# Performance work log

Hardware: AMD Instinct MI355X
Metric: run time of the kernel (lower is better)

## Reference

```python
import jax, jax.numpy as jnp
import numpy as np

EPS = 1e-6  # mmdet bbox_overlaps eps


def _nearest_bev(boxes7):
    # boxes7: [N, 7] = (x, y, z, dx, dy, dz, yaw). LiDARInstance3DBoxes.nearest_bev:
    # limit yaw to [-pi/2, pi/2) via limit_period(yaw, 0.5, pi); if |yaw| > pi/4 swap dx/dy,
    # then return axis-aligned (x1, y1, x2, y2).
    x, y = boxes7[:, 0], boxes7[:, 1]
    dx, dy = boxes7[:, 3], boxes7[:, 4]
    yaw = boxes7[:, 6]
    pi = jnp.float32(np.pi)
    normed = jnp.abs(yaw - jnp.floor(yaw / pi + 0.5) * pi)
    swap = normed > pi / 4
    w = jnp.where(swap, dy, dx)
    h = jnp.where(swap, dx, dy)
    return jnp.stack([x - w / 2, y - h / 2, x + w / 2, y + h / 2], axis=-1)


def _pairwise_iou(b):
    # b: [N, 4] x1y1x2y2 -> [N, N] IoU (mmdet bbox_overlaps, mode='iou')
    area = (b[:, 2] - b[:, 0]) * (b[:, 3] - b[:, 1])
    lt = jnp.maximum(b[:, None, :2], b[None, :, :2])
    rb = jnp.minimum(b[:, None, 2:], b[None, :, 2:])
    wh = jnp.clip(rb - lt, 0.0)
    inter = wh[..., 0] * wh[..., 1]
    union = jnp.maximum(area[:, None] + area[None, :] - inter, EPS)
    return inter / union


def setup_inputs() -> dict:
    key = jax.random.key(0)
    k1, k2, k3, k4, k5, k6 = jax.random.split(key, 6)
    B, A, C, H, W, box_dim = 2, 2, 10, 32, 32, 7
    N = H * W * A
    scores = jax.random.normal(k1, (B, A * C, H, W), jnp.float32)
    bbox_preds = jax.random.normal(k2, (B, A * box_dim, H, W), jnp.float32)
    pp_params = jax.random.normal(k3, (B, C * 3, H, W), jnp.float32)
    centers = jax.random.uniform(k4, (B, N, 3), jnp.float32, 0.0, 50.0)
    sizes = jax.random.uniform(k5, (B, N, 3), jnp.float32, 1.0, 5.0)
    yaw = jax.random.uniform(k6, (B, N, 1), jnp.float32, -np.pi, np.pi)
    decoded = jnp.concatenate([centers, sizes, yaw], axis=-1)  # [B, N, 7]
    return {"scores": scores, "bbox_preds": bbox_preds, "pp_params": pp_params, "decoded": decoded}


def reference(scores, bbox_preds, pp_params, decoded):
    B, AC, H, W = scores.shape
    N = decoded.shape[1]
    A = N // (H * W)
    C = AC // A
    # flatten_scores: (B,A,C,H,W) -> (B,H,W,A,C) -> (B, HWA, C)
    sc_f = scores.reshape(B, A, C, H, W).transpose(0, 3, 4, 1, 2).reshape(B, N, C)
    # flatten_pp: (B,C,3,H,W) -> (B,H,W,C,3), broadcast over A -> (B, HWA, C, 3)
    pp_hw = pp_params.reshape(B, C, 3, H, W).transpose(0, 3, 4, 1, 2)  # [B,H,W,C,3]
    pp_f = jnp.broadcast_to(pp_hw[:, :, :, None, :, :], (B, H, W, A, C, 3)).reshape(B, N, C, 3)
    # per-batch BEV IoU matrices
    bev = jax.vmap(_nearest_bev)(decoded[..., :7])        # [B, N, 4]
    iou = jax.vmap(_pairwise_iou)(bev)                    # [B, N, N]
    # per-class outer-product bias + row softmax + matmul with column softmax of scores
    p0 = pp_f[..., 0]                                     # [B, N, C]
    p1 = pp_f[..., 1]                                     # [B, N, C]
    bias = p0[:, :, None, :] * p1[:, None, :, :]          # [B, N, N, C]
    weight = jax.nn.softmax(iou[..., None] + bias, axis=2)  # softmax over keys (dim=1 of NxN)
    sm_sc = jax.nn.softmax(sc_f, axis=1)                  # softmax over N per class
    new_sc = jnp.einsum('bnmc,bmc->bnc', weight, sm_sc)   # [B, N, C]
    # un-flatten back to level layout: (B,H,W,A,C) -> (B, A*C, H, W)
    out_scores = new_sc.reshape(B, H, W, A, C).transpose(0, 3, 4, 1, 2).reshape(B, A * C, H, W)
    return out_scores, bbox_preds, pp_params
```

## Files before the change

kernel.cpp:

```cpp
#include <hip/hip_runtime.h>
#include <math.h>

#define Bz 2
#define Az 2
#define Cz 10
#define HWz 1024
#define Nz 2048
#define ACHW (Az*Cz*HWz)
#define NBBOX (Bz*Az*7*HWz)
#define NPP   (Bz*Cz*3*HWz)
#define EPSf 1e-6f
#define LOG2E 1.4426950408889634f

#if __has_builtin(__builtin_amdgcn_exp2f)
#define EXP2F(x) __builtin_amdgcn_exp2f(x)
#else
#define EXP2F(x) exp2f(x)
#endif
#if __has_builtin(__builtin_amdgcn_rcpf)
#define RCPF(x) __builtin_amdgcn_rcpf(x)
#else
#define RCPF(x) (1.0f/(x))
#endif

static __device__ __forceinline__ unsigned short f2bf(float x) {
    unsigned u = __builtin_bit_cast(unsigned, x);
    unsigned r = (u + 0x7fffu + ((u >> 16) & 1u)) >> 16;
    return (unsigned short)r;
}

#if __has_builtin(__builtin_amdgcn_update_dpp)
static __device__ __forceinline__ float wred(float x) {
    int t;
    t = __builtin_amdgcn_update_dpp(0, __builtin_bit_cast(int, x), 0x111, 0xf, 0xf, true);
    x += __builtin_bit_cast(float, t);
    t = __builtin_amdgcn_update_dpp(0, __builtin_bit_cast(int, x), 0x112, 0xf, 0xf, true);
    x += __builtin_bit_cast(float, t);
    t = __builtin_amdgcn_update_dpp(0, __builtin_bit_cast(int, x), 0x114, 0xf, 0xf, true);
    x += __builtin_bit_cast(float, t);
    t = __builtin_amdgcn_update_dpp(0, __builtin_bit_cast(int, x), 0x118, 0xf, 0xf, true);
    x += __builtin_bit_cast(float, t);
    t = __builtin_amdgcn_update_dpp(0, __builtin_bit_cast(int, x), 0x142, 0xa, 0xf, true);
    x += __builtin_bit_cast(float, t);
    t = __builtin_amdgcn_update_dpp(0, __builtin_bit_cast(int, x), 0x143, 0xc, 0xf, true);
    x += __builtin_bit_cast(float, t);
    return x;
}
#define WRED_LANE 63
#else
static __device__ __forceinline__ float wred(float x) {
    for (int off = 32; off > 0; off >>= 1) x += __shfl_down(x, off);
    return x;
}
#define WRED_LANE 0
#endif

static __device__ __forceinline__ float iou_e(float nx1,float ny1,float nx2,float ny2,float ar,
                                              float mx1,float my1,float mx2,float my2,float am) {
    float xx1 = fmaxf(nx1, mx1), yy1 = fmaxf(ny1, my1);
    float xx2 = fminf(nx2, mx2), yy2 = fminf(ny2, my2);
    float iw = fmaxf(xx2 - xx1, 0.f), ih = fmaxf(yy2 - yy1, 0.f);
    float inter = iw * ih;
    float uni = fmaxf(ar + am - inter, EPSf);
    return EXP2F(inter * LOG2E * RCPF(uni));
}


__global__ __launch_bounds__(256) void k_pre(const float* __restrict__ scores,
                                             const float* __restrict__ bbox,
                                             const float* __restrict__ pp,
                                             const float* __restrict__ dec,
                                             float* __restrict__ out,
                                             float2* __restrict__ LT,
                                             float2* __restrict__ RB,
                                             uint2* __restrict__ PQ,
                                             float* __restrict__ Z) {
    int blk = blockIdx.x;
    int tid = threadIdx.x;

    if (blk < 240) {
        int i = blk * 256 + tid;
        if (i < NBBOX) out[Bz*ACHW + i] = bbox[i];
        if (i < NPP)   out[Bz*ACHW + NBBOX + i] = pp[i];
        return;
    }
    if (blk < 256) {
        int i = (blk - 240) * 256 + tid;
        const float* d = dec + i*7;
        float x = d[0], y = d[1], dx = d[3], dy = d[4], yaw = d[6];
        const float PI = 3.14159265358979323846f;
        float normed = fabsf(yaw - floorf(yaw/PI + 0.5f) * PI);
        bool swp = normed > PI * 0.25f;
        float w = swp ? dy : dx;
        float h = swp ? dx : dy;
        LT[i] = make_float2(x - 0.5f*w, y - 0.5f*h);
        RB[i] = make_float2(x + 0.5f*w, y + 0.5f*h);
        return;
    }
    __shared__ float SV[Nz];
    __shared__ float ws4[4];
    int wave = tid >> 6, lane = tid & 63;
    int bc = blk - 256;
    int b = bc / Cz, c = bc % Cz;
    const float* sbase = scores + b*ACHW + c*HWz;
    float sum = 0.f;
    #pragma unroll
    for (int j = 0; j < Nz/256; j++) {
        int n = tid + (j << 8);
        int a = n & 1, hw = n >> 1;
        float e = EXP2F(sbase[a*(Cz*HWz) + hw] * LOG2E);
        sum += e;
        SV[n] = e;
    }
    #pragma unroll
    for (int off = 32; off > 0; off >>= 1) sum += __shfl_xor(sum, off);
    if (lane == 0) ws4[wave] = sum;
    __syncthreads();
    if (tid == 0) Z[b*Cz + c] = ws4[0] + ws4[1] + ws4[2] + ws4[3];
    const float* p1base = pp + b*(Cz*3*HWz) + (c*3 + 1)*HWz;
    uint2* gp = PQ + ((size_t)b << 10) * Cz + c;
    #pragma unroll
    for (int k = 0; k < 4; k++) {
        int hm = tid + (k << 8);
        unsigned qq = (unsigned)f2bf(SV[2*hm]) | ((unsigned)f2bf(SV[2*hm + 1]) << 16);
        float p1 = p1base[hm] * LOG2E;
        gp[(size_t)hm * Cz] = make_uint2(__builtin_bit_cast(unsigned, p1), qq);
    }
}

#define PROC(P1BITS, QQ, c) { \
    float p1_ = __builtin_bit_cast(float, (P1BITS)); \
    float q0_ = __builtin_bit_cast(float, (QQ) << 16); \
    float q1_ = __builtin_bit_cast(float, (QQ) & 0xffff0000u); \
    float F_ = EXP2F(p0[c] * p1_); \
    l0[c] = fmaf(F_, S0, l0[c]); \
    l1[c] = fmaf(F_, S1, l1[c]); \
    float t0_ = fmaf(E01, q1_, E00 * q0_); \
    float t1_ = fmaf(E11, q1_, E10 * q0_); \
    a0[c] = fmaf(F_, t0_, a0[c]); \
    a1[c] = fmaf(F_, t1_, a1[c]); }

__global__ __launch_bounds__(256, 4) void k_main(const float4* __restrict__ LT4,
                                                 const float4* __restrict__ RB4,
                                                 const uint4* __restrict__ PQ4,
                                                 const float* __restrict__ pp,
                                                 const float* __restrict__ Z,
                                                 float* __restrict__ out) {
    __shared__ float SRED[2][2][40];

    int tid = threadIdx.x;
    int wave = tid >> 6, lane = tid & 63;
    int hl = wave >> 1;
    int s  = wave & 1;
    int bid = blockIdx.x;
    int b = bid >> 9;
    int g = bid & 511;
    int hn = (g << 1) + hl;
    int mb = s << 9;

    const float4* LTb = LT4 + (b << 10);
    const float4* RBb = RB4 + (b << 10);
    const uint4*  PQb = PQ4 + ((size_t)(b << 10)) * 5;

    float4 bx = LTb[hn];
    float4 by = RBb[hn];
    float ar0 = (by.x - bx.x) * (by.y - bx.y);
    float ar1 = (by.z - bx.z) * (by.w - bx.w);

    float p0[Cz];
    const float* p0base = pp + b*(Cz*3*HWz) + hn;
    #pragma unroll
    for (int c = 0; c < Cz; c++) p0[c] = p0base[c * 3 * HWz];

    float l0[Cz], l1[Cz], a0[Cz], a1[Cz];
    #pragma unroll
    for (int c = 0; c < Cz; c++) { l0[c]=0.f; l1[c]=0.f; a0[c]=0.f; a1[c]=0.f; }

    for (int t = 0; t < 8; ++t) {
        int hm = mb + (t << 6) + lane;
        float4 bl = LTb[hm];
        float4 br = RBb[hm];
        const uint4* qp = PQb + (size_t)hm * 5;
        uint4 r0 = qp[0], r1 = qp[1], r2 = qp[2], r3 = qp[3], r4 = qp[4];

        float am0 = (br.x - bl.x) * (br.y - bl.y);
        float am1 = (br.z - bl.z) * (br.w - bl.w);
        float E00 = iou_e(bx.x,bx.y,by.x,by.y,ar0, bl.x,bl.y,br.x,br.y,am0);
        float E01 = iou_e(bx.x,bx.y,by.x,by.y,ar0, bl.z,bl.w,br.z,br.w,am1);
        float E10 = iou_e(bx.z,bx.w,by.z,by.w,ar1, bl.x,bl.y,br.x,br.y,am0);
        float E11 = iou_e(bx.z,bx.w,by.z,by.w,ar1, bl.z,bl.w,br.z,br.w,am1);
        float S0 = E00 + E01, S1 = E10 + E11;

        PROC(r0.x, r0.y, 0) PROC(r0.z, r0.w, 1)
        PROC(r1.x, r1.y, 2) PROC(r1.z, r1.w, 3)
        PROC(r2.x, r2.y, 4) PROC(r2.z, r2.w, 5)
        PROC(r3.x, r3.y, 6) PROC(r3.z, r3.w, 7)
        PROC(r4.x, r4.y, 8) PROC(r4.z, r4.w, 9)
    }

    #pragma unroll
    for (int c = 0; c < Cz; c++) {
        l0[c] = wred(l0[c]); l1[c] = wred(l1[c]);
        a0[c] = wred(a0[c]); a1[c] = wred(a1[c]);
    }
    if (lane == WRED_LANE) {
        #pragma unroll
        for (int c = 0; c < Cz; c++) {
            SRED[hl][s][c]      = l0[c];
            SRED[hl][s][10 + c] = l1[c];
            SRED[hl][s][20 + c] = a0[c];
            SRED[hl][s][30 + c] = a1[c];
        }
    }
    __syncthreads();
    if (tid < 40) {
        int h   = tid >= 20 ? 1 : 0;
        int idx = tid - 20*h;
        int r   = idx >= 10 ? 1 : 0;
        int c   = idx - 10*r;
        float den = (SRED[h][0][idx] + SRED[h][1][idx]) * Z[b*Cz + c];
        float num =  SRED[h][0][20 + idx] + SRED[h][1][20 + idx];
        int hh = (g << 1) + h;
        out[b*ACHW + (r*Cz + c)*HWz + hh] = num * RCPF(den);
    }
}

extern "C" void kernel_launch(void* const* d_in, const int* in_sizes, int n_in,
                              void* d_out, int out_size, void* d_ws, size_t ws_size,
                              hipStream_t stream) {
    const float* scores = (const float*)d_in[0];
    const float* bbox   = (const float*)d_in[1];
    const float* pp     = (const float*)d_in[2];
    const float* dec    = (const float*)d_in[3];
    float* out = (float*)d_out;

    float2* LT = (float2*)d_ws;
    float2* RB = LT + (size_t)Bz*Nz;
    uint2*  PQ = (uint2*)(RB + (size_t)Bz*Nz);
    float*  Z  = (float*)(PQ + (size_t)Bz*HWz*Cz);

    hipLaunchKernelGGL(k_pre,  dim3(276), dim3(256), 0, stream,
                       scores, bbox, pp, dec, out, LT, RB, PQ, Z);
    hipLaunchKernelGGL(k_main, dim3(1024), dim3(256), 0, stream,
                       (const float4*)LT, (const float4*)RB, (const uint4*)PQ, pp, Z, out);
}
```

Measured before the change: 76.95 us.

## Process two query cells per wave with SoA PQ layout and software-prefetched key loads

Each wave now handles two query HW cells instead of one, so every loaded key tile (boxes and packed p1/score values) is reused across twice as many queries, and the grid is halved to 512 blocks. The PQ workspace is changed from an interleaved per-cell layout to a class-pair-major structure-of-arrays, so consecutive lanes read consecutive uint4s (coalesced). Key tile loads are double-buffered across the unrolled loop so the next tile is in flight while the current one is computed. The cost is roughly double the accumulator registers, and the occupancy hint in launch_bounds is dropped, which may lower occupancy or cause spills.

```diff
diff --git a/kernel.cpp b/kernel.cpp
--- a/kernel.cpp
+++ b/kernel.cpp
@@ -118,109 +118,144 @@
     __syncthreads();
     if (tid == 0) Z[b*Cz + c] = ws4[0] + ws4[1] + ws4[2] + ws4[3];
     const float* p1base = pp + b*(Cz*3*HWz) + (c*3 + 1)*HWz;
-    uint2* gp = PQ + ((size_t)b << 10) * Cz + c;
+    uint2* gp = PQ + (((size_t)b*5 + (c >> 1)) * HWz) * 2 + (c & 1);
     #pragma unroll
     for (int k = 0; k < 4; k++) {
         int hm = tid + (k << 8);
         unsigned qq = (unsigned)f2bf(SV[2*hm]) | ((unsigned)f2bf(SV[2*hm + 1]) << 16);
         float p1 = p1base[hm] * LOG2E;
-        gp[(size_t)hm * Cz] = make_uint2(__builtin_bit_cast(unsigned, p1), qq);
-    }
-}
-
-#define PROC(P1BITS, QQ, c) { \
+        gp[2*hm] = make_uint2(__builtin_bit_cast(unsigned, p1), qq);
+    }
+}
+
+
+#define LOADM(t, BL, BR, Q0, Q1, Q2, Q3, Q4) { \
+    int hm_ = mb + ((t) << 6) + lane; \
+    BL = LTb[hm_]; BR = RBb[hm_]; \
+    Q0 = PQb[hm_]; Q1 = PQb[HWz + hm_]; Q2 = PQb[2*HWz + hm_]; \
+    Q3 = PQb[3*HWz + hm_]; Q4 = PQb[4*HWz + hm_]; }
+
+#define PROC2(P1BITS, QQ, c) { \
     float p1_ = __builtin_bit_cast(float, (P1BITS)); \
     float q0_ = __builtin_bit_cast(float, (QQ) << 16); \
     float q1_ = __builtin_bit_cast(float, (QQ) & 0xffff0000u); \
-    float F_ = EXP2F(p0[c] * p1_); \
-    l0[c] = fmaf(F_, S0, l0[c]); \
-    l1[c] = fmaf(F_, S1, l1[c]); \
-    float t0_ = fmaf(E01, q1_, E00 * q0_); \
-    float t1_ = fmaf(E11, q1_, E10 * q0_); \
-    a0[c] = fmaf(F_, t0_, a0[c]); \
-    a1[c] = fmaf(F_, t1_, a1[c]); }
-
-__global__ __launch_bounds__(256, 4) void k_main(const float4* __restrict__ LT4,
-                                                 const float4* __restrict__ RB4,
-                                                 const uint4* __restrict__ PQ4,
-                                                 const float* __restrict__ pp,
-                                                 const float* __restrict__ Z,
-                                                 float* __restrict__ out) {
-    __shared__ float SRED[2][2][40];
+    float FA_ = EXP2F(p0A[c] * p1_); \
+    float FB_ = EXP2F(p0B[c] * p1_); \
+    lA0[c] = fmaf(FA_, SA0, lA0[c]); lA1[c] = fmaf(FA_, SA1, lA1[c]); \
+    lB0[c] = fmaf(FB_, SB0, lB0[c]); lB1[c] = fmaf(FB_, SB1, lB1[c]); \
+    float t0A_ = fmaf(EA01, q1_, EA00 * q0_); \
+    float t1A_ = fmaf(EA11, q1_, EA10 * q0_); \
+    float t0B_ = fmaf(EB01, q1_, EB00 * q0_); \
+    float t1B_ = fmaf(EB11, q1_, EB10 * q0_); \
+    aA0[c] = fmaf(FA_, t0A_, aA0[c]); aA1[c] = fmaf(FA_, t1A_, aA1[c]); \
+    aB0[c] = fmaf(FB_, t0B_, aB0[c]); aB1[c] = fmaf(FB_, t1B_, aB1[c]); }
+
+#define COMP(BL, BR, Q0, Q1, Q2, Q3, Q4) { \
+    float am0 = (BR.x - BL.x) * (BR.y - BL.y); \
+    float am1 = (BR.z - BL.z) * (BR.w - BL.w); \
+    float EA00 = iou_e(bxA.x,bxA.y,byA.x,byA.y,arA0, BL.x,BL.y,BR.x,BR.y,am0); \
+    float EA01 = iou_e(bxA.x,bxA.y,byA.x,byA.y,arA0, BL.z,BL.w,BR.z,BR.w,am1); \
+    float EA10 = iou_e(bxA.z,bxA.w,byA.z,byA.w,arA1, BL.x,BL.y,BR.x,BR.y,am0); \
+    float EA11 = iou_e(bxA.z,bxA.w,byA.z,byA.w,arA1, BL.z,BL.w,BR.z,BR.w,am1); \
+    float EB00 = iou_e(bxB.x,bxB.y,byB.x,byB.y,arB0, BL.x,BL.y,BR.x,BR.y,am0); \
+    float EB01 = iou_e(bxB.x,bxB.y,byB.x,byB.y,arB0, BL.z,BL.w,BR.z,BR.w,am1); \
+    float EB10 = iou_e(bxB.z,bxB.w,byB.z,byB.w,arB1, BL.x,BL.y,BR.x,BR.y,am0); \
+    float EB11 = iou_e(bxB.z,bxB.w,byB.z,byB.w,arB1, BL.z,BL.w,BR.z,BR.w,am1); \
+    float SA0 = EA00 + EA01, SA1 = EA10 + EA11; \
+    float SB0 = EB00 + EB01, SB1 = EB10 + EB11; \
+    PROC2(Q0.x, Q0.y, 0) PROC2(Q0.z, Q0.w, 1) \
+    PROC2(Q1.x, Q1.y, 2) PROC2(Q1.z, Q1.w, 3) \
+    PROC2(Q2.x, Q2.y, 4) PROC2(Q2.z, Q2.w, 5) \
+    PROC2(Q3.x, Q3.y, 6) PROC2(Q3.z, Q3.w, 7) \
+    PROC2(Q4.x, Q4.y, 8) PROC2(Q4.z, Q4.w, 9) }
+
+__global__ __launch_bounds__(256) void k_main(const float4* __restrict__ LT4,
+                                              const float4* __restrict__ RB4,
+                                              const uint4* __restrict__ PQ4,
+                                              const float* __restrict__ pp,
+                                              const float* __restrict__ Z,
+                                              float* __restrict__ out) {
+    __shared__ float SRED[2][2][80];
 
     int tid = threadIdx.x;
     int wave = tid >> 6, lane = tid & 63;
     int hl = wave >> 1;
     int s  = wave & 1;
     int bid = blockIdx.x;
-    int b = bid >> 9;
-    int g = bid & 511;
-    int hn = (g << 1) + hl;
+    int b = bid >> 8;
+    int g = bid & 255;
+    int hnA = (g << 2) + (hl << 1);
     int mb = s << 9;
 
     const float4* LTb = LT4 + (b << 10);
     const float4* RBb = RB4 + (b << 10);
-    const uint4*  PQb = PQ4 + ((size_t)(b << 10)) * 5;
-
-    float4 bx = LTb[hn];
-    float4 by = RBb[hn];
-    float ar0 = (by.x - bx.x) * (by.y - bx.y);
-    float ar1 = (by.z - bx.z) * (by.w - bx.w);
-
-    float p0[Cz];
-    const float* p0base = pp + b*(Cz*3*HWz) + hn;
-    #pragma unroll
-    for (int c = 0; c < Cz; c++) p0[c] = p0base[c * 3 * HWz];
-
-    float l0[Cz], l1[Cz], a0[Cz], a1[Cz];
-    #pragma unroll
-    for (int c = 0; c < Cz; c++) { l0[c]=0.f; l1[c]=0.f; a0[c]=0.f; a1[c]=0.f; }
-
-    for (int t = 0; t < 8; ++t) {
-        int hm = mb + (t << 6) + lane;
-        float4 bl = LTb[hm];
-        float4 br = RBb[hm];
-        const uint4* qp = PQb + (size_t)hm * 5;
-        uint4 r0 = qp[0], r1 = qp[1], r2 = qp[2], r3 = qp[3], r4 = qp[4];
-
-        float am0 = (br.x - bl.x) * (br.y - bl.y);
-        float am1 = (br.z - bl.z) * (br.w - bl.w);
-        float E00 = iou_e(bx.x,bx.y,by.x,by.y,ar0, bl.x,bl.y,br.x,br.y,am0);
-        float E01 = iou_e(bx.x,bx.y,by.x,by.y,ar0, bl.z,bl.w,br.z,br.w,am1);
-        float E10 = iou_e(bx.z,bx.w,by.z,by.w,ar1, bl.x,bl.y,br.x,br.y,am0);
-        float E11 = iou_e(bx.z,bx.w,by.z,by.w,ar1, bl.z,bl.w,br.z,br.w,am1);
-        float S0 = E00 + E01, S1 = E10 + E11;
-
-        PROC(r0.x, r0.y, 0) PROC(r0.z, r0.w, 1)
-        PROC(r1.x, r1.y, 2) PROC(r1.z, r1.w, 3)
-        PROC(r2.x, r2.y, 4) PROC(r2.z, r2.w, 5)
-        PROC(r3.x, r3.y, 6) PROC(r3.z, r3.w, 7)
-        PROC(r4.x, r4.y, 8) PROC(r4.z, r4.w, 9)
-    }
-
+    const uint4*  PQb = PQ4 + (size_t)b * 5 * HWz;
+
+    float4 bxA = LTb[hnA],     byA = RBb[hnA];
+    float4 bxB = LTb[hnA + 1], byB = RBb[hnA + 1];
+    float arA0 = (byA.x - bxA.x) * (byA.y - bxA.y);
+    float arA1 = (byA.z - bxA.z) * (byA.w - bxA.w);
+    float arB0 = (byB.x - bxB.x) * (byB.y - bxB.y);
+    float arB1 = (byB.z - bxB.z) * (byB.w - bxB.w);
+
+    float p0A[Cz], p0B[Cz];
+    const float* p0base = pp + b*(Cz*3*HWz);
     #pragma unroll
     for (int c = 0; c < Cz; c++) {
-        l0[c] = wred(l0[c]); l1[c] = wred(l1[c]);
-        a0[c] = wred(a0[c]); a1[c] = wred(a1[c]);
+        p0A[c] = p0base[c * 3 * HWz + hnA];
+        p0B[c] = p0base[c * 3 * HWz + hnA + 1];
+    }
+
+    float lA0[Cz], lA1[Cz], lB0[Cz], lB1[Cz];
+    float aA0[Cz], aA1[Cz], aB0[Cz], aB1[Cz];
+    #pragma unroll
+    for (int c = 0; c < Cz; c++) {
+        lA0[c]=0.f; lA1[c]=0.f; lB0[c]=0.f; lB1[c]=0.f;
+        aA0[c]=0.f; aA1[c]=0.f; aB0[c]=0.f; aB1[c]=0.f;
+    }
+
+    float4 pblA, pbrA, pblB, pbrB;
+    uint4 pqA0, pqA1, pqA2, pqA3, pqA4, pqB0, pqB1, pqB2, pqB3, pqB4;
+
+    LOADM(0, pblA, pbrA, pqA0, pqA1, pqA2, pqA3, pqA4)
+    #pragma unroll
+    for (int t = 0; t < 8; t += 2) {
+        if (t + 1 < 8) LOADM(t + 1, pblB, pbrB, pqB0, pqB1, pqB2, pqB3, pqB4)
+        COMP(pblA, pbrA, pqA0, pqA1, pqA2, pqA3, pqA4)
+        if (t + 2 < 8) LOADM(t + 2, pblA, pbrA, pqA0, pqA1, pqA2, pqA3, pqA4)
+        COMP(pblB, pbrB, pqB0, pqB1, pqB2, pqB3, pqB4)
+    }
+
+    #pragma unroll
+    for (int c = 0; c < Cz; c++) {
+        lA0[c] = wred(lA0[c]); lA1[c] = wred(lA1[c]);
+        lB0[c] = wred(lB0[c]); lB1[c] = wred(lB1[c]);
+        aA0[c] = wred(aA0[c]); aA1[c] = wred(aA1[c]);
+        aB0[c] = wred(aB0[c]); aB1[c] = wred(aB1[c]);
     }
     if (lane == WRED_LANE) {
         #pragma unroll
         for (int c = 0; c < Cz; c++) {
-            SRED[hl][s][c]      = l0[c];
-            SRED[hl][s][10 + c] = l1[c];
-            SRED[hl][s][20 + c] = a0[c];
-            SRED[hl][s][30 + c] = a1[c];
+            SRED[hl][s][c]      = lA0[c];
+            SRED[hl][s][10 + c] = lA1[c];
+            SRED[hl][s][20 + c] = lB0[c];
+            SRED[hl][s][30 + c] = lB1[c];
+            SRED[hl][s][40 + c] = aA0[c];
+            SRED[hl][s][50 + c] = aA1[c];
+            SRED[hl][s][60 + c] = aB0[c];
+            SRED[hl][s][70 + c] = aB1[c];
         }
     }
     __syncthreads();
-    if (tid < 40) {
-        int h   = tid >= 20 ? 1 : 0;
-        int idx = tid - 20*h;
-        int r   = idx >= 10 ? 1 : 0;
-        int c   = idx - 10*r;
-        float den = (SRED[h][0][idx] + SRED[h][1][idx]) * Z[b*Cz + c];
-        float num =  SRED[h][0][20 + idx] + SRED[h][1][20 + idx];
-        int hh = (g << 1) + h;
+    if (tid < 80) {
+        int h   = tid / 20;
+        int rem = tid - 20*h;
+        int r   = rem / 10;
+        int c   = rem - 10*r;
+        int idx = ((h & 1) * 2 + r) * 10 + c;
+        float den = (SRED[h >> 1][0][idx] + SRED[h >> 1][1][idx]) * Z[b*Cz + c];
+        float num =  SRED[h >> 1][0][40 + idx] + SRED[h >> 1][1][40 + idx];
+        int hh = (g << 2) + h;
         out[b*ACHW + (r*Cz + c)*HWz + hh] = num * RCPF(den);
     }
 }
@@ -237,10 +272,10 @@
     float2* LT = (float2*)d_ws;
     float2* RB = LT + (size_t)Bz*Nz;
     uint2*  PQ = (uint2*)(RB + (size_t)Bz*Nz);
-    float*  Z  = (float*)(PQ + (size_t)Bz*HWz*Cz);
+    float*  Z  = (float*)(PQ + (size_t)Bz*5*HWz*2);
 
     hipLaunchKernelGGL(k_pre,  dim3(276), dim3(256), 0, stream,
                        scores, bbox, pp, dec, out, LT, RB, PQ, Z);
-    hipLaunchKernelGGL(k_main, dim3(1024), dim3(256), 0, stream,
+    hipLaunchKernelGGL(k_main, dim3(512), dim3(256), 0, stream,
                        (const float4*)LT, (const float4*)RB, (const uint4*)PQ, pp, Z, out);
 }
```

Result: slower. 92.04 us (+19.6%).

## Fuse pre and main kernels into one cooperative launch with grid sync

Applied to the files above, without the earlier changes.

Merges the preprocessing kernel and the main attention kernel into a single cooperative kernel that separates the phases with a grid-wide barrier. The aim is to remove the second kernel launch and the gap between the two dispatches. If the cooperative launch fails, it falls back to the original two launches. The trade-offs are the cost of the grid sync, the extra shared memory that every block now reserves for both phases, and the requirement that all 1024 blocks be co-resident.

```diff
diff --git a/kernel.cpp b/kernel.cpp
--- a/kernel.cpp
+++ b/kernel.cpp
@@ -1,5 +1,8 @@
 #include <hip/hip_runtime.h>
+#include <hip/hip_cooperative_groups.h>
 #include <math.h>
+
+namespace cg = cooperative_groups;
 
 #define Bz 2
 #define Az 2
@@ -66,18 +69,17 @@
 }
 
 
-__global__ __launch_bounds__(256) void k_pre(const float* __restrict__ scores,
-                                             const float* __restrict__ bbox,
-                                             const float* __restrict__ pp,
-                                             const float* __restrict__ dec,
-                                             float* __restrict__ out,
-                                             float2* __restrict__ LT,
-                                             float2* __restrict__ RB,
-                                             uint2* __restrict__ PQ,
-                                             float* __restrict__ Z) {
-    int blk = blockIdx.x;
-    int tid = threadIdx.x;
-
+static __device__ __forceinline__ void prep_body(int blk, int tid,
+                                                 const float* __restrict__ scores,
+                                                 const float* __restrict__ bbox,
+                                                 const float* __restrict__ pp,
+                                                 const float* __restrict__ dec,
+                                                 float* __restrict__ out,
+                                                 float2* __restrict__ LT,
+                                                 float2* __restrict__ RB,
+                                                 uint2* __restrict__ PQ,
+                                                 float* __restrict__ Z,
+                                                 float* SV, float* ws4) {
     if (blk < 240) {
         int i = blk * 256 + tid;
         if (i < NBBOX) out[Bz*ACHW + i] = bbox[i];
@@ -97,8 +99,7 @@
         RB[i] = make_float2(x + 0.5f*w, y + 0.5f*h);
         return;
     }
-    __shared__ float SV[Nz];
-    __shared__ float ws4[4];
+    if (blk >= 276) return;
     int wave = tid >> 6, lane = tid & 63;
     int bc = blk - 256;
     int b = bc / Cz, c = bc % Cz;
@@ -140,19 +141,17 @@
     a0[c] = fmaf(F_, t0_, a0[c]); \
     a1[c] = fmaf(F_, t1_, a1[c]); }
 
-__global__ __launch_bounds__(256, 4) void k_main(const float4* __restrict__ LT4,
+static __device__ __forceinline__ void main_body(int bid, int tid,
+                                                 const float4* __restrict__ LT4,
                                                  const float4* __restrict__ RB4,
                                                  const uint4* __restrict__ PQ4,
                                                  const float* __restrict__ pp,
                                                  const float* __restrict__ Z,
-                                                 float* __restrict__ out) {
-    __shared__ float SRED[2][2][40];
-
-    int tid = threadIdx.x;
+                                                 float* __restrict__ out,
+                                                 float (*SRED)[2][40]) {
     int wave = tid >> 6, lane = tid & 63;
     int hl = wave >> 1;
     int s  = wave & 1;
-    int bid = blockIdx.x;
     int b = bid >> 9;
     int g = bid & 511;
     int hn = (g << 1) + hl;
@@ -225,6 +224,50 @@
     }
 }
 
+__global__ __launch_bounds__(256, 4) void k_fused(const float* __restrict__ scores,
+                                                  const float* __restrict__ bbox,
+                                                  const float* __restrict__ pp,
+                                                  const float* __restrict__ dec,
+                                                  float* __restrict__ out,
+                                                  float2* __restrict__ LT,
+                                                  float2* __restrict__ RB,
+                                                  uint2* __restrict__ PQ,
+                                                  float* __restrict__ Z) {
+    __shared__ float SV[Nz];
+    __shared__ float ws4[4];
+    __shared__ float SRED[2][2][40];
+    int blk = blockIdx.x, tid = threadIdx.x;
+
+    prep_body(blk, tid, scores, bbox, pp, dec, out, LT, RB, PQ, Z, SV, ws4);
+    cg::this_grid().sync();
+    main_body(blk, tid, (const float4*)LT, (const float4*)RB, (const uint4*)PQ,
+              pp, Z, out, SRED);
+}
+
+__global__ __launch_bounds__(256) void k_pre(const float* __restrict__ scores,
+                                             const float* __restrict__ bbox,
+                                             const float* __restrict__ pp,
+                                             const float* __restrict__ dec,
+                                             float* __restrict__ out,
+                                             float2* __restrict__ LT,
+                                             float2* __restrict__ RB,
+                                             uint2* __restrict__ PQ,
+                                             float* __restrict__ Z) {
+    __shared__ float SV[Nz];
+    __shared__ float ws4[4];
+    prep_body(blockIdx.x, threadIdx.x, scores, bbox, pp, dec, out, LT, RB, PQ, Z, SV, ws4);
+}
+
+__global__ __launch_bounds__(256, 4) void k_main(const float4* __restrict__ LT4,
+                                                 const float4* __restrict__ RB4,
+                                                 const uint4* __restrict__ PQ4,
+                                                 const float* __restrict__ pp,
+                                                 const float* __restrict__ Z,
+                                                 float* __restrict__ out) {
+    __shared__ float SRED[2][2][40];
+    main_body(blockIdx.x, threadIdx.x, LT4, RB4, PQ4, pp, Z, out, SRED);
+}
+
 extern "C" void kernel_launch(void* const* d_in, const int* in_sizes, int n_in,
                               void* d_out, int out_size, void* d_ws, size_t ws_size,
                               hipStream_t stream) {
@@ -239,8 +282,14 @@
     uint2*  PQ = (uint2*)(RB + (size_t)Bz*Nz);
     float*  Z  = (float*)(PQ + (size_t)Bz*HWz*Cz);
 
-    hipLaunchKernelGGL(k_pre,  dim3(276), dim3(256), 0, stream,
-                       scores, bbox, pp, dec, out, LT, RB, PQ, Z);
-    hipLaunchKernelGGL(k_main, dim3(1024), dim3(256), 0, stream,
-                       (const float4*)LT, (const float4*)RB, (const uint4*)PQ, pp, Z, out);
-}
+    void* args[] = { (void*)&scores, (void*)&bbox, (void*)&pp, (void*)&dec,
+                     (void*)&out, (void*)&LT, (void*)&RB, (void*)&PQ, (void*)&Z };
+    hipError_t e = hipLaunchCooperativeKernel((const void*)k_fused,
+                                              dim3(1024), dim3(256), args, 0, stream);
+    if (e != hipSuccess) {
+        hipLaunchKernelGGL(k_pre,  dim3(276), dim3(256), 0, stream,
+                           scores, bbox, pp, dec, out, LT, RB, PQ, Z);
+        hipLaunchKernelGGL(k_main, dim3(1024), dim3(256), 0, stream,
+                           (const float4*)LT, (const float4*)RB, (const uint4*)PQ, pp, Z, out);
+    }
+}
```

Result: slower. 202.3 us (+163.0%).

## Move passthrough copy into main kernel, relayout PQ, double-buffer key loads

Applied to the files above, without the earlier changes.

The bbox/pp passthrough copy moves out of the preprocess kernel into the main kernel, with each block copying 88 elements. This cuts k_pre from 276 to 36 blocks. PQ is laid out class-pair-major so that main-kernel loads of each class pair are coalesced across lanes. k_pre also drops its shared-memory staging. The key loop is fully unrolled with register double-buffering of the next tile's loads, and launch bounds drop to 2 blocks/CU, trading occupancy for more registers.

```diff
diff --git a/kernel.cpp b/kernel.cpp
--- a/kernel.cpp
+++ b/kernel.cpp
@@ -67,10 +67,8 @@
 
 
 __global__ __launch_bounds__(256) void k_pre(const float* __restrict__ scores,
-                                             const float* __restrict__ bbox,
                                              const float* __restrict__ pp,
                                              const float* __restrict__ dec,
-                                             float* __restrict__ out,
                                              float2* __restrict__ LT,
                                              float2* __restrict__ RB,
                                              uint2* __restrict__ PQ,
@@ -78,14 +76,8 @@
     int blk = blockIdx.x;
     int tid = threadIdx.x;
 
-    if (blk < 240) {
+    if (blk < 16) {
         int i = blk * 256 + tid;
-        if (i < NBBOX) out[Bz*ACHW + i] = bbox[i];
-        if (i < NPP)   out[Bz*ACHW + NBBOX + i] = pp[i];
-        return;
-    }
-    if (blk < 256) {
-        int i = (blk - 240) * 256 + tid;
         const float* d = dec + i*7;
         float x = d[0], y = d[1], dx = d[3], dy = d[4], yaw = d[6];
         const float PI = 3.14159265358979323846f;
@@ -97,35 +89,30 @@
         RB[i] = make_float2(x + 0.5f*w, y + 0.5f*h);
         return;
     }
-    __shared__ float SV[Nz];
     __shared__ float ws4[4];
     int wave = tid >> 6, lane = tid & 63;
-    int bc = blk - 256;
+    int bc = blk - 16;
     int b = bc / Cz, c = bc % Cz;
-    const float* sbase = scores + b*ACHW + c*HWz;
+    const float* s0p = scores + b*ACHW + c*HWz;
+    const float* s1p = s0p + Cz*HWz;
+    const float* p1base = pp + b*(Cz*3*HWz) + (c*3 + 1)*HWz;
+    uint2* gp = PQ + ((size_t)(b*5 + (c >> 1)) * HWz) * 2 + (c & 1);
     float sum = 0.f;
     #pragma unroll
-    for (int j = 0; j < Nz/256; j++) {
-        int n = tid + (j << 8);
-        int a = n & 1, hw = n >> 1;
-        float e = EXP2F(sbase[a*(Cz*HWz) + hw] * LOG2E);
-        sum += e;
-        SV[n] = e;
+    for (int j = 0; j < 4; j++) {
+        int hw = tid + (j << 8);
+        float e0 = EXP2F(s0p[hw] * LOG2E);
+        float e1 = EXP2F(s1p[hw] * LOG2E);
+        sum += e0 + e1;
+        unsigned qq = (unsigned)f2bf(e0) | ((unsigned)f2bf(e1) << 16);
+        float p1 = p1base[hw] * LOG2E;
+        gp[2*hw] = make_uint2(__builtin_bit_cast(unsigned, p1), qq);
     }
     #pragma unroll
     for (int off = 32; off > 0; off >>= 1) sum += __shfl_xor(sum, off);
     if (lane == 0) ws4[wave] = sum;
     __syncthreads();
     if (tid == 0) Z[b*Cz + c] = ws4[0] + ws4[1] + ws4[2] + ws4[3];
-    const float* p1base = pp + b*(Cz*3*HWz) + (c*3 + 1)*HWz;
-    uint2* gp = PQ + ((size_t)b << 10) * Cz + c;
-    #pragma unroll
-    for (int k = 0; k < 4; k++) {
-        int hm = tid + (k << 8);
-        unsigned qq = (unsigned)f2bf(SV[2*hm]) | ((unsigned)f2bf(SV[2*hm + 1]) << 16);
-        float p1 = p1base[hm] * LOG2E;
-        gp[(size_t)hm * Cz] = make_uint2(__builtin_bit_cast(unsigned, p1), qq);
-    }
 }
 
 #define PROC(P1BITS, QQ, c) { \
@@ -140,10 +127,31 @@
     a0[c] = fmaf(F_, t0_, a0[c]); \
     a1[c] = fmaf(F_, t1_, a1[c]); }
 
-__global__ __launch_bounds__(256, 4) void k_main(const float4* __restrict__ LT4,
+#define LOADM(t, BL, BR, Q0, Q1, Q2, Q3, Q4) { \
+    int hm_ = mb + ((t) << 6) + lane; \
+    BL = LTb[hm_]; BR = RBb[hm_]; \
+    Q0 = PQb[hm_]; Q1 = PQb[HWz + hm_]; Q2 = PQb[2*HWz + hm_]; \
+    Q3 = PQb[3*HWz + hm_]; Q4 = PQb[4*HWz + hm_]; }
+
+#define COMP(BL, BR, Q0, Q1, Q2, Q3, Q4) { \
+    float am0 = (BR.x - BL.x) * (BR.y - BL.y); \
+    float am1 = (BR.z - BL.z) * (BR.w - BL.w); \
+    float E00 = iou_e(bx.x,bx.y,by.x,by.y,ar0, BL.x,BL.y,BR.x,BR.y,am0); \
+    float E01 = iou_e(bx.x,bx.y,by.x,by.y,ar0, BL.z,BL.w,BR.z,BR.w,am1); \
+    float E10 = iou_e(bx.z,bx.w,by.z,by.w,ar1, BL.x,BL.y,BR.x,BR.y,am0); \
+    float E11 = iou_e(bx.z,bx.w,by.z,by.w,ar1, BL.z,BL.w,BR.z,BR.w,am1); \
+    float S0 = E00 + E01, S1 = E10 + E11; \
+    PROC(Q0.x, Q0.y, 0) PROC(Q0.z, Q0.w, 1) \
+    PROC(Q1.x, Q1.y, 2) PROC(Q1.z, Q1.w, 3) \
+    PROC(Q2.x, Q2.y, 4) PROC(Q2.z, Q2.w, 5) \
+    PROC(Q3.x, Q3.y, 6) PROC(Q3.z, Q3.w, 7) \
+    PROC(Q4.x, Q4.y, 8) PROC(Q4.z, Q4.w, 9) }
+
+__global__ __launch_bounds__(256, 2) void k_main(const float4* __restrict__ LT4,
                                                  const float4* __restrict__ RB4,
                                                  const uint4* __restrict__ PQ4,
                                                  const float* __restrict__ pp,
+                                                 const float* __restrict__ bbox,
                                                  const float* __restrict__ Z,
                                                  float* __restrict__ out) {
     __shared__ float SRED[2][2][40];
@@ -158,9 +166,17 @@
     int hn = (g << 1) + hl;
     int mb = s << 9;
 
+    {
+        int i = bid * 88 + tid;
+        if (tid < 88) {
+            float v = (i < NBBOX) ? bbox[i] : pp[i - NBBOX];
+            out[Bz*ACHW + i] = v;
+        }
+    }
+
     const float4* LTb = LT4 + (b << 10);
     const float4* RBb = RB4 + (b << 10);
-    const uint4*  PQb = PQ4 + ((size_t)(b << 10)) * 5;
+    const uint4*  PQb = PQ4 + (size_t)b * 5 * HWz;
 
     float4 bx = LTb[hn];
     float4 by = RBb[hn];
@@ -176,26 +192,16 @@
     #pragma unroll
     for (int c = 0; c < Cz; c++) { l0[c]=0.f; l1[c]=0.f; a0[c]=0.f; a1[c]=0.f; }
 
-    for (int t = 0; t < 8; ++t) {
-        int hm = mb + (t << 6) + lane;
-        float4 bl = LTb[hm];
-        float4 br = RBb[hm];
-        const uint4* qp = PQb + (size_t)hm * 5;
-        uint4 r0 = qp[0], r1 = qp[1], r2 = qp[2], r3 = qp[3], r4 = qp[4];
-
-        float am0 = (br.x - bl.x) * (br.y - bl.y);
-        float am1 = (br.z - bl.z) * (br.w - bl.w);
-        float E00 = iou_e(bx.x,bx.y,by.x,by.y,ar0, bl.x,bl.y,br.x,br.y,am0);
-        float E01 = iou_e(bx.x,bx.y,by.x,by.y,ar0, bl.z,bl.w,br.z,br.w,am1);
-        float E10 = iou_e(bx.z,bx.w,by.z,by.w,ar1, bl.x,bl.y,br.x,br.y,am0);
-        float E11 = iou_e(bx.z,bx.w,by.z,by.w,ar1, bl.z,bl.w,br.z,br.w,am1);
-        float S0 = E00 + E01, S1 = E10 + E11;
-
-        PROC(r0.x, r0.y, 0) PROC(r0.z, r0.w, 1)
-        PROC(r1.x, r1.y, 2) PROC(r1.z, r1.w, 3)
-        PROC(r2.x, r2.y, 4) PROC(r2.z, r2.w, 5)
-        PROC(r3.x, r3.y, 6) PROC(r3.z, r3.w, 7)
-        PROC(r4.x, r4.y, 8) PROC(r4.z, r4.w, 9)
+    float4 blA, brA, blB, brB;
+    uint4 qA0, qA1, qA2, qA3, qA4, qB0, qB1, qB2, qB3, qB4;
+
+    LOADM(0, blA, brA, qA0, qA1, qA2, qA3, qA4)
+    #pragma unroll
+    for (int t = 0; t < 8; t += 2) {
+        LOADM(t + 1, blB, brB, qB0, qB1, qB2, qB3, qB4)
+        COMP(blA, brA, qA0, qA1, qA2, qA3, qA4)
+        if (t + 2 < 8) LOADM(t + 2, blA, brA, qA0, qA1, qA2, qA3, qA4)
+        COMP(blB, brB, qB0, qB1, qB2, qB3, qB4)
     }
 
     #pragma unroll
@@ -237,10 +243,11 @@
     float2* LT = (float2*)d_ws;
     float2* RB = LT + (size_t)Bz*Nz;
     uint2*  PQ = (uint2*)(RB + (size_t)Bz*Nz);
-    float*  Z  = (float*)(PQ + (size_t)Bz*HWz*Cz);
-
-    hipLaunchKernelGGL(k_pre,  dim3(276), dim3(256), 0, stream,
-                       scores, bbox, pp, dec, out, LT, RB, PQ, Z);
+    float*  Z  = (float*)(PQ + (size_t)Bz*5*HWz*2);
+
+    hipLaunchKernelGGL(k_pre,  dim3(36), dim3(256), 0, stream,
+                       scores, pp, dec, LT, RB, PQ, Z);
     hipLaunchKernelGGL(k_main, dim3(1024), dim3(256), 0, stream,
-                       (const float4*)LT, (const float4*)RB, (const uint4*)PQ, pp, Z, out);
-}
+                       (const float4*)LT, (const float4*)RB, (const uint4*)PQ,
+                       pp, bbox, Z, out);
+}
```

Measured after the change: 77.58 us. No clear change (+0.8%).
